# Kernel tuning notes

Measured on AMD Instinct MI355X. Metric: run time of the kernel, lower is better.

## Reference

```python
import jax, jax.numpy as jnp
import numpy as np


def _conv1x1(x, w, b):
    # x: (B,C,H,W), w: (O,C), b: (O,)  == nn.Conv2d(C,O,kernel_size=1)
    return jnp.einsum('bchw,oc->bohw', x, w) + b[None, :, None, None]


def _maxpool2(x):
    # MaxPool2d(kernel_size=2, stride=2) on NCHW
    return jax.lax.reduce_window(x, -jnp.inf, jax.lax.max,
                                 (1, 1, 2, 2), (1, 1, 2, 2), 'VALID')


def setup_inputs() -> dict:
    key = jax.random.key(0)
    ks = jax.random.split(key, 10)
    B, C, H, W = 16, 256, 64, 64
    Cs = C // 8  # channel_split = 8 -> 32
    s = 1.0 / np.sqrt(C)  # keep softmax logits well-scaled
    return {
        'x': jax.random.normal(ks[0], (B, C, H, W), dtype=jnp.float32),
        'wq': jax.random.normal(ks[1], (Cs, C), dtype=jnp.float32) * s,
        'bq': jnp.zeros((Cs,), dtype=jnp.float32),
        'wk': jax.random.normal(ks[2], (Cs, C), dtype=jnp.float32) * s,
        'bk': jnp.zeros((Cs,), dtype=jnp.float32),
        'wv': jax.random.normal(ks[3], (C, C), dtype=jnp.float32) * s,
        'bv': jnp.zeros((C,), dtype=jnp.float32),
        'wo': jax.random.normal(ks[4], (C, C), dtype=jnp.float32) * s,
        'bo': jnp.zeros((C,), dtype=jnp.float32),
        'gamma': jnp.ones((1,), dtype=jnp.float32),
    }


def reference(x, wq, bq, wk, bk, wv, bv, wo, bo, gamma):
    B, C, H, W = x.shape
    # Q: conv -> maxpool -> flatten -> (B, Np, C')
    q = _maxpool2(_conv1x1(x, wq, bq))
    Np = q.shape[2] * q.shape[3]
    q = q.reshape(B, -1, Np).transpose(0, 2, 1)          # (B, Np, C')
    # K: conv -> flatten -> (B, C', N)
    k = _conv1x1(x, wk, bk).reshape(B, -1, H * W)        # (B, C', N)
    energy = jnp.einsum('bnc,bcm->bnm', q, k)            # (B, Np, N)
    attention = jax.nn.softmax(energy, axis=-1)
    # V: conv -> maxpool -> flatten -> (B, C, Np)
    v = _maxpool2(_conv1x1(x, wv, bv)).reshape(B, C, Np)
    out = jnp.einsum('bcn,bnm->bcm', v, attention)       # (B, C, N)
    out = out.reshape(B, C, H, W)
    out = _conv1x1(out, wo, bo)
    return gamma * out + x
```

## Files before the change

### kernel.cpp

```cpp
#include <hip/hip_runtime.h>
#include <math.h>

#define Bb 16
#define Cn 256
#define Cs 32
#define Nn 4096
#define Np 1024
#define Ww 64
#define MS2 16

#define MT 64
#define NT2 128
#define PR2 (NT2 + 8)

#define PO 136
#define QKPAD 36

typedef __attribute__((ext_vector_type(8))) short short8;
typedef __attribute__((ext_vector_type(4))) float f32x4;

__device__ inline short f2bf(float f) {
    unsigned u = __builtin_bit_cast(unsigned, f);
    u += 0x7fff + ((u >> 16) & 1);
    return (short)(u >> 16);
}
__device__ inline float bf2f(short s) {
    unsigned u = ((unsigned)(unsigned short)s) << 16;
    return __builtin_bit_cast(float, u);
}
__device__ inline unsigned bfmax4(unsigned u0, unsigned u1, unsigned u2, unsigned u3) {
    float l = fmaxf(fmaxf(__builtin_bit_cast(float, u0 << 16),
                          __builtin_bit_cast(float, u1 << 16)),
                    fmaxf(__builtin_bit_cast(float, u2 << 16),
                          __builtin_bit_cast(float, u3 << 16)));
    float h = fmaxf(fmaxf(__builtin_bit_cast(float, u0 & 0xffff0000u),
                          __builtin_bit_cast(float, u1 & 0xffff0000u)),
                    fmaxf(__builtin_bit_cast(float, u2 & 0xffff0000u),
                          __builtin_bit_cast(float, u3 & 0xffff0000u)));
    return (__builtin_bit_cast(unsigned, h) & 0xffff0000u) |
           (__builtin_bit_cast(unsigned, l) >> 16);
}

__global__ void tobf_k(const float* __restrict__ in, short* __restrict__ out, int n) {
    int idx = blockIdx.x * 256 + threadIdx.x;
    if (idx < n) out[idx] = f2bf(in[idx]);
}

__global__ __launch_bounds__(256) void xpose_bf(const float* __restrict__ x,
                                                short* __restrict__ xbfT) {
    __shared__ float T[64][65];
    int lane = threadIdx.x & 63, g = threadIdx.x >> 6;
    int b = blockIdx.z, c0 = blockIdx.y * 64, m0 = blockIdx.x * 64;
    const float* xb = x + ((size_t)b * Cn + c0) * Nn + m0;
#pragma unroll
    for (int r = 0; r < 16; ++r) {
        int c_l = r * 4 + g;
        T[c_l][lane] = xb[(size_t)c_l * Nn + lane];
    }
    __syncthreads();
    short* ob = xbfT + ((size_t)b * Nn + m0) * Cn + c0;
#pragma unroll
    for (int r = 0; r < 16; ++r) {
        int m_l = r * 4 + g;
        ob[(size_t)m_l * Cn + lane] = f2bf(T[lane][m_l]);
    }
}

__global__ __launch_bounds__(256) void conv_qk_mfma(
    const short* __restrict__ xbfT, const short* __restrict__ wqBf,
    const short* __restrict__ wkBf, const float* __restrict__ bq,
    const float* __restrict__ bk, short* __restrict__ KT,
    short* __restrict__ QpT) {
    __shared__ short Tq[128 * QKPAD];
    int lane = threadIdx.x & 63;
    int wave = __builtin_amdgcn_readfirstlane(threadIdx.x >> 6);
    int l16 = lane & 15, quad = lane >> 4;
    int b = blockIdx.y;
    int h = blockIdx.x;
    int m0 = h * 128 + (wave >> 1) * 64;
    int isK = wave & 1;
    const short* wB = isK ? wkBf : wqBf;
    const float* bias = isK ? bk : bq;
    const short* Arow = wB + (size_t)l16 * Cn + quad * 8;
    const short* Brow = xbfT + ((size_t)b * Nn + m0 + l16) * Cn + quad * 8;
    f32x4 acc[2][4];
#pragma unroll
    for (int i = 0; i < 2; ++i)
#pragma unroll
        for (int j = 0; j < 4; ++j) acc[i][j] = (f32x4){0.f, 0.f, 0.f, 0.f};
    for (int kk = 0; kk < Cn; kk += 32) {
        short8 af[2], bf[4];
#pragma unroll
        for (int fo = 0; fo < 2; ++fo)
            af[fo] = *(const short8*)(Arow + (size_t)(fo * 16) * Cn + kk);
#pragma unroll
        for (int fm = 0; fm < 4; ++fm)
            bf[fm] = *(const short8*)(Brow + (size_t)(fm * 16) * Cn + kk);
#pragma unroll
        for (int fo = 0; fo < 2; ++fo)
#pragma unroll
            for (int fm = 0; fm < 4; ++fm)
                acc[fo][fm] = __builtin_amdgcn_mfma_f32_16x16x32_bf16(
                    af[fo], bf[fm], acc[fo][fm], 0, 0, 0);
    }
#pragma unroll
    for (int fo = 0; fo < 2; ++fo) {
        int c0 = fo * 16 + quad * 4;
        float b0 = bias[c0], b1 = bias[c0 + 1], b2 = bias[c0 + 2], b3 = bias[c0 + 3];
#pragma unroll
        for (int fm = 0; fm < 4; ++fm) {
            int m_rel = (wave >> 1) * 64 + fm * 16 + l16;
            unsigned lo = ((unsigned)(unsigned short)f2bf(acc[fo][fm][1] + b1) << 16) |
                          (unsigned short)f2bf(acc[fo][fm][0] + b0);
            unsigned hi = ((unsigned)(unsigned short)f2bf(acc[fo][fm][3] + b3) << 16) |
                          (unsigned short)f2bf(acc[fo][fm][2] + b2);
            if (isK) {
                int m = h * 128 + m_rel;
                *(uint2*)&KT[((size_t)b * Nn + m) * Cs + c0] = make_uint2(lo, hi);
            } else {
                *(uint2*)&Tq[m_rel * QKPAD + c0] = make_uint2(lo, hi);
            }
        }
    }
    __syncthreads();
    int pw = threadIdx.x >> 3;
    int cs = (threadIdx.x & 7) * 4;
    uint2 A0 = *(const uint2*)&Tq[(2 * pw) * QKPAD + cs];
    uint2 A1 = *(const uint2*)&Tq[(2 * pw + 1) * QKPAD + cs];
    uint2 A2 = *(const uint2*)&Tq[(64 + 2 * pw) * QKPAD + cs];
    uint2 A3 = *(const uint2*)&Tq[(64 + 2 * pw + 1) * QKPAD + cs];
    unsigned w0 = bfmax4(A0.x, A1.x, A2.x, A3.x);
    unsigned w1 = bfmax4(A0.y, A1.y, A2.y, A3.y);
    *(uint2*)&QpT[((size_t)b * Np + h * 32 + pw) * Cs + cs] = make_uint2(w0, w1);
}

__global__ __launch_bounds__(256) void conv_v_pool(
    const short* __restrict__ xbfT, const short* __restrict__ wvBf,
    const float* __restrict__ bv, short* __restrict__ VpT) {
    __shared__ short T[128 * PO];
    int lane = threadIdx.x & 63;
    int wave = __builtin_amdgcn_readfirstlane(threadIdx.x >> 6);
    int l16 = lane & 15, quad = lane >> 4;
    int b = blockIdx.z;
    int h = blockIdx.x;
    int m0 = h * 128 + (wave >> 1) * 64;
    int o0 = blockIdx.y * 128 + (wave & 1) * 64;
    const short* Arow = wvBf + (size_t)(o0 + l16) * Cn + quad * 8;
    const short* Brow = xbfT + ((size_t)b * Nn + m0 + l16) * Cn + quad * 8;
    f32x4 acc[4][4];
#pragma unroll
    for (int i = 0; i < 4; ++i)
#pragma unroll
        for (int j = 0; j < 4; ++j) acc[i][j] = (f32x4){0.f, 0.f, 0.f, 0.f};
    for (int kk = 0; kk < Cn; kk += 32) {
        short8 af[4], bf[4];
#pragma unroll
        for (int fo = 0; fo < 4; ++fo)
            af[fo] = *(const short8*)(Arow + (size_t)(fo * 16) * Cn + kk);
#pragma unroll
        for (int fm = 0; fm < 4; ++fm)
            bf[fm] = *(const short8*)(Brow + (size_t)(fm * 16) * Cn + kk);
#pragma unroll
        for (int fo = 0; fo < 4; ++fo)
#pragma unroll
            for (int fm = 0; fm < 4; ++fm)
                acc[fo][fm] = __builtin_amdgcn_mfma_f32_16x16x32_bf16(
                    af[fo], bf[fm], acc[fo][fm], 0, 0, 0);
    }
#pragma unroll
    for (int fo = 0; fo < 4; ++fo) {
        int o_loc = (wave & 1) * 64 + fo * 16 + quad * 4;
        int o_g = blockIdx.y * 128 + o_loc;
        float b0 = bv[o_g], b1 = bv[o_g + 1], b2 = bv[o_g + 2], b3 = bv[o_g + 3];
#pragma unroll
        for (int fm = 0; fm < 4; ++fm) {
            int m_rel = (wave >> 1) * 64 + fm * 16 + l16;
            unsigned lo = ((unsigned)(unsigned short)f2bf(acc[fo][fm][1] + b1) << 16) |
                          (unsigned short)f2bf(acc[fo][fm][0] + b0);
            unsigned hi = ((unsigned)(unsigned short)f2bf(acc[fo][fm][3] + b3) << 16) |
                          (unsigned short)f2bf(acc[fo][fm][2] + b2);
            *(uint2*)&T[m_rel * PO + o_loc] = make_uint2(lo, hi);
        }
    }
    __syncthreads();
#pragma unroll
    for (int rep = 0; rep < 2; ++rep) {
        int t = threadIdx.x + rep * 256;
        int cg = t & 15;
        int pw = t >> 4;
        const short* r0 = &T[(2 * pw) * PO + cg * 8];
        const short* r1 = r0 + PO;
        const short* r2 = &T[(64 + 2 * pw) * PO + cg * 8];
        const short* r3 = r2 + PO;
        short8 a = *(const short8*)r0, b8 = *(const short8*)r1;
        short8 c8 = *(const short8*)r2, d8 = *(const short8*)r3;
        short8 o8;
#pragma unroll
        for (int j = 0; j < 8; ++j) {
            float v = fmaxf(fmaxf(bf2f(a[j]), bf2f(b8[j])),
                            fmaxf(bf2f(c8[j]), bf2f(d8[j])));
            o8[j] = f2bf(v);
        }
        int n = h * 32 + pw;
        *(short8*)(VpT + ((size_t)b * Np + n) * Cn + blockIdx.y * 128 + cg * 8) = o8;
    }
}

__global__ __launch_bounds__(256) void vo_mfma(
    const short* __restrict__ VpT, const short* __restrict__ woBf,
    short* __restrict__ VoBf) {
    int lane = threadIdx.x & 63;
    int wave = __builtin_amdgcn_readfirstlane(threadIdx.x >> 6);
    int l16 = lane & 15, quad = lane >> 4;
    int b = blockIdx.z;
    int n0 = blockIdx.x * 128 + (wave >> 1) * 64;
    int o0 = blockIdx.y * 128 + (wave & 1) * 64;
    const short* Arow = woBf + (size_t)(o0 + l16) * Cn + quad * 8;
    const short* Brow = VpT + ((size_t)b * Np + n0 + l16) * Cn + quad * 8;
    f32x4 acc[4][4];
#pragma unroll
    for (int i = 0; i < 4; ++i)
#pragma unroll
        for (int j = 0; j < 4; ++j) acc[i][j] = (f32x4){0.f, 0.f, 0.f, 0.f};
    for (int kk = 0; kk < Cn; kk += 32) {
        short8 af[4], bf[4];
#pragma unroll
        for (int fo = 0; fo < 4; ++fo)
            af[fo] = *(const short8*)(Arow + (size_t)(fo * 16) * Cn + kk);
#pragma unroll
        for (int fm = 0; fm < 4; ++fm)
            bf[fm] = *(const short8*)(Brow + (size_t)(fm * 16) * Cn + kk);
#pragma unroll
        for (int fo = 0; fo < 4; ++fo)
#pragma unroll
            for (int fm = 0; fm < 4; ++fm)
                acc[fo][fm] = __builtin_amdgcn_mfma_f32_16x16x32_bf16(
                    af[fo], bf[fm], acc[fo][fm], 0, 0, 0);
    }
#pragma unroll
    for (int fo = 0; fo < 4; ++fo)
#pragma unroll
        for (int fm = 0; fm < 4; ++fm) {
            int n = n0 + fm * 16 + l16;
#pragma unroll
            for (int r = 0; r < 4; ++r) {
                int o = o0 + fo * 16 + quad * 4 + r;
                VoBf[((size_t)b * Cn + o) * Np + n] = f2bf(acc[fo][fm][r]);
            }
        }
}

__global__ __launch_bounds__(256) void rowstats_mfma(
    const short* __restrict__ KT, const short* __restrict__ QpT,
    float* __restrict__ pS) {
    int lane = threadIdx.x & 63;
    int wave = __builtin_amdgcn_readfirstlane(threadIdx.x >> 6);
    int l16 = lane & 15, quad = lane >> 4;
    int b = blockIdx.y, ms = blockIdx.z;
    int nbase = blockIdx.x * 256 + wave * 64;
    short8 af[4];
#pragma unroll
    for (int nf = 0; nf < 4; ++nf)
        af[nf] = *(const short8*)(QpT +
            ((size_t)b * Np + nbase + nf * 16 + l16) * Cs + quad * 8);
    float Sv[4][4];
#pragma unroll
    for (int nf = 0; nf < 4; ++nf)
#pragma unroll
        for (int r = 0; r < 4; ++r) Sv[nf][r] = 0.f;
    int m0 = ms * (Nn / MS2);
    for (int mm = 0; mm < Nn / MS2; mm += 16) {
        short8 bf = *(const short8*)(KT +
            ((size_t)b * Nn + m0 + mm + l16) * Cs + quad * 8);
#pragma unroll
        for (int nf = 0; nf < 4; ++nf) {
            f32x4 e = __builtin_amdgcn_mfma_f32_16x16x32_bf16(
                af[nf], bf, (f32x4){0.f, 0.f, 0.f, 0.f}, 0, 0, 0);
#pragma unroll
            for (int r = 0; r < 4; ++r)
                Sv[nf][r] += __expf(e[r] - 20.f);
        }
    }
#pragma unroll
    for (int nf = 0; nf < 4; ++nf)
#pragma unroll
        for (int r = 0; r < 4; ++r) {
            float S = Sv[nf][r];
#pragma unroll
            for (int s = 1; s <= 8; s <<= 1) S += __shfl_xor(S, s);
            Sv[nf][r] = S;
        }
    if (l16 == 0) {
#pragma unroll
        for (int nf = 0; nf < 4; ++nf)
#pragma unroll
            for (int r = 0; r < 4; ++r) {
                size_t o = ((size_t)ms * Bb + b) * Np + nbase + nf * 16 +
                           quad * 4 + r;
                pS[o] = Sv[nf][r];
            }
    }
}

__global__ void comb_k(const float* __restrict__ pS, float* __restrict__ Ae) {
    int gidx = blockIdx.x * 256 + threadIdx.x;
    int b = gidx >> 10, n = gidx & (Np - 1);
    float S = 0.f;
#pragma unroll
    for (int ms = 0; ms < MS2; ++ms)
        S += pS[((size_t)ms * Bb + b) * Np + n];
    Ae[(size_t)b * Np + n] = 20.f + __logf(S);
}

__global__ __launch_bounds__(512) void attn_out_k(
    const short* __restrict__ KT, const short* __restrict__ QpT,
    const short* __restrict__ VoBf, const float* __restrict__ Ae,
    const float* __restrict__ bo, const float* __restrict__ gamma,
    const float* __restrict__ x, float* __restrict__ out) {
    __shared__ short P[2][MT * PR2];
    int tid  = threadIdx.x;
    int lane = tid & 63;
    int wave = __builtin_amdgcn_readfirstlane(tid >> 6);
    int l16 = lane & 15, quad = lane >> 4;
    int b  = blockIdx.y;
    int m0 = blockIdx.x * MT;

    const short* QT = QpT + (size_t)b * Np * Cs;
    const short* Kb = KT + ((size_t)b * Nn + m0) * Cs;
    const short* Vb = VoBf + ((size_t)b * Cn + wave * 32) * Np;
    const float* Ab = Ae + (size_t)b * Np;

    short8 kf[4];
#pragma unroll
    for (int mf = 0; mf < 4; ++mf)
        kf[mf] = *(const short8*)(Kb + (size_t)(mf * 16 + l16) * Cs + quad * 8);

    f32x4 acc[2][4];
#pragma unroll
    for (int i = 0; i < 2; ++i)
#pragma unroll
        for (int j = 0; j < 4; ++j) acc[i][j] = (f32x4){0.f, 0.f, 0.f, 0.f};

    auto Ephase = [&](int t) {
        int buf = t & 1;
        int nb = t * NT2 + wave * 16;
        short8 qf = *(const short8*)(QT + (size_t)(nb + l16) * Cs + quad * 8);
        f32x4 av = *(const f32x4*)&Ab[nb + quad * 4];
#pragma unroll
        for (int mf = 0; mf < 4; ++mf) {
            f32x4 e = __builtin_amdgcn_mfma_f32_16x16x32_bf16(
                qf, kf[mf], (f32x4){0.f, 0.f, 0.f, 0.f}, 0, 0, 0);
            float p0 = __expf(e[0] - av[0]);
            float p1 = __expf(e[1] - av[1]);
            float p2 = __expf(e[2] - av[2]);
            float p3 = __expf(e[3] - av[3]);
            unsigned p01 = ((unsigned)(unsigned short)f2bf(p1) << 16) |
                           (unsigned short)f2bf(p0);
            unsigned p23 = ((unsigned)(unsigned short)f2bf(p3) << 16) |
                           (unsigned short)f2bf(p2);
            int m_l = mf * 16 + l16;
            int n_l = wave * 16 + quad * 4;
            *(uint2*)&P[buf][m_l * PR2 + n_l] = make_uint2(p01, p23);
        }
    };

    Ephase(0);
    __syncthreads();
    for (int t = 0; t < 8; ++t) {
        if (t < 7) Ephase(t + 1);
        const short* At = Vb + t * NT2;
        int buf = t & 1;
#pragma unroll
        for (int kk = 0; kk < NT2; kk += 32) {
            short8 bfr[4], afr[2];
#pragma unroll
            for (int fm = 0; fm < 4; ++fm)
                bfr[fm] = *(const short8*)&P[buf][(fm * 16 + l16) * PR2 + kk + quad * 8];
#pragma unroll
            for (int fo = 0; fo < 2; ++fo)
                afr[fo] = *(const short8*)(At + (size_t)(fo * 16 + l16) * Np +
                                           kk + quad * 8);
#pragma unroll
            for (int fo = 0; fo < 2; ++fo)
#pragma unroll
                for (int fm = 0; fm < 4; ++fm)
                    acc[fo][fm] = __builtin_amdgcn_mfma_f32_16x16x32_bf16(
                        afr[fo], bfr[fm], acc[fo][fm], 0, 0, 0);
        }
        __syncthreads();
    }
    float g = gamma[0];
#pragma unroll
    for (int fo = 0; fo < 2; ++fo)
#pragma unroll
        for (int fm = 0; fm < 4; ++fm) {
            int m = m0 + fm * 16 + l16;
#pragma unroll
            for (int r = 0; r < 4; ++r) {
                int o = wave * 32 + fo * 16 + quad * 4 + r;
                size_t idx = ((size_t)b * Cn + o) * Nn + m;
                out[idx] = g * (acc[fo][fm][r] + bo[o]) + x[idx];
            }
        }
}

extern "C" void kernel_launch(void* const* d_in, const int* in_sizes, int n_in,
                              void* d_out, int out_size, void* d_ws, size_t ws_size,
                              hipStream_t stream) {
    (void)in_sizes; (void)n_in; (void)out_size; (void)ws_size;
    const float* x     = (const float*)d_in[0];
    const float* wq    = (const float*)d_in[1];
    const float* bq    = (const float*)d_in[2];
    const float* wk    = (const float*)d_in[3];
    const float* bk    = (const float*)d_in[4];
    const float* wv    = (const float*)d_in[5];
    const float* bv    = (const float*)d_in[6];
    const float* wo    = (const float*)d_in[7];
    const float* bo    = (const float*)d_in[8];
    const float* gamma = (const float*)d_in[9];
    float* out = (float*)d_out;

    float* ws = (float*)d_ws;
    size_t off = 0;
    short* xbfT = (short*)(ws + off); off += (size_t)Bb * Nn * Cn / 2;
    short* VpT  = (short*)(ws + off); off += (size_t)Bb * Np * Cn / 2;
    short* VoBf = (short*)(ws + off); off += (size_t)Bb * Cn * Np / 2;
    short* KT   = (short*)(ws + off); off += (size_t)Bb * Nn * Cs / 2;
    short* QpT  = (short*)(ws + off); off += (size_t)Bb * Np * Cs / 2;
    float* pS   = ws + off;           off += (size_t)MS2 * Bb * Np;
    float* Ae   = ws + off;           off += (size_t)Bb * Np;
    short* wqBf = (short*)(ws + off); off += (size_t)Cs * Cn / 2;
    short* wkBf = (short*)(ws + off); off += (size_t)Cs * Cn / 2;
    short* wvBf = (short*)(ws + off); off += (size_t)Cn * Cn / 2;
    short* woBf = (short*)(ws + off); off += (size_t)Cn * Cn / 2;

    tobf_k<<<dim3((Cs * Cn + 255) / 256), 256, 0, stream>>>(wq, wqBf, Cs * Cn);
    tobf_k<<<dim3((Cs * Cn + 255) / 256), 256, 0, stream>>>(wk, wkBf, Cs * Cn);
    tobf_k<<<dim3(Cn * Cn / 256), 256, 0, stream>>>(wv, wvBf, Cn * Cn);
    tobf_k<<<dim3(Cn * Cn / 256), 256, 0, stream>>>(wo, woBf, Cn * Cn);

    xpose_bf<<<dim3(Nn / 64, Cn / 64, Bb), 256, 0, stream>>>(x, xbfT);

    conv_qk_mfma<<<dim3(Nn / 128, Bb), 256, 0, stream>>>(xbfT, wqBf, wkBf,
                                                         bq, bk, KT, QpT);

    conv_v_pool<<<dim3(Nn / 128, Cn / 128, Bb), 256, 0, stream>>>(xbfT, wvBf, bv, VpT);

    rowstats_mfma<<<dim3(Np / 256, Bb, MS2), 256, 0, stream>>>(KT, QpT, pS);
    comb_k<<<dim3(Bb * Np / 256), 256, 0, stream>>>(pS, Ae);

    vo_mfma<<<dim3(Np / 128, Cn / 128, Bb), 256, 0, stream>>>(VpT, woBf, VoBf);

    attn_out_k<<<dim3(Nn / MT, Bb), 512, 0, stream>>>(KT, QpT, VoBf, Ae,
                                                      bo, gamma, x, out);
}
```

Before: 284.4 us.

## Merge independent launches, fold log2e into Wq, use exp2 and packed bf16 converts

Four weight-conversion kernels are merged into one launch. The Q/K and V convolutions now run in a single grid dispatched by block index, and so do rowstats and vo_mfma. This removes launch gaps and lets independent work share the device. Wq and bq are prescaled by log2(e) so softmax can use the hardware exp2/log2 instructions, and float-to-bf16 packing uses v_cvt_pk_bf16_f32. Rounding from prescaling Wq in bf16 changes numerics slightly.

```diff
diff --git a/kernel.cpp b/kernel.cpp
--- a/kernel.cpp
+++ b/kernel.cpp
@@ -16,8 +16,14 @@
 #define PO 136
 #define QKPAD 36
 
+#define C20L 28.8539008f
+#define L2E  1.44269504f
+
 typedef __attribute__((ext_vector_type(8))) short short8;
 typedef __attribute__((ext_vector_type(4))) float f32x4;
+
+__device__ inline float fexp2(float x) { return __builtin_amdgcn_exp2f(x); }
+__device__ inline float flog2(float x) { return __builtin_amdgcn_logf(x); }
 
 __device__ inline short f2bf(float f) {
     unsigned u = __builtin_bit_cast(unsigned, f);
@@ -27,6 +33,11 @@
 __device__ inline float bf2f(short s) {
     unsigned u = ((unsigned)(unsigned short)s) << 16;
     return __builtin_bit_cast(float, u);
+}
+__device__ inline unsigned pk2bf(float lo, float hi) {
+    unsigned r;
+    asm("v_cvt_pk_bf16_f32 %0, %1, %2" : "=v"(r) : "v"(lo), "v"(hi));
+    return r;
 }
 __device__ inline unsigned bfmax4(unsigned u0, unsigned u1, unsigned u2, unsigned u3) {
     float l = fmaxf(fmaxf(__builtin_bit_cast(float, u0 << 16),
@@ -41,9 +52,15 @@
            (__builtin_bit_cast(unsigned, l) >> 16);
 }
 
-__global__ void tobf_k(const float* __restrict__ in, short* __restrict__ out, int n) {
+__global__ void wprep_k(const float* __restrict__ wq, const float* __restrict__ wk,
+                        const float* __restrict__ wv, const float* __restrict__ wo,
+                        short* __restrict__ wqBf, short* __restrict__ wkBf,
+                        short* __restrict__ wvBf, short* __restrict__ woBf) {
     int idx = blockIdx.x * 256 + threadIdx.x;
-    if (idx < n) out[idx] = f2bf(in[idx]);
+    if (idx < 8192)        wqBf[idx] = f2bf(wq[idx] * L2E);
+    else if (idx < 16384)  wkBf[idx - 8192] = f2bf(wk[idx - 8192]);
+    else if (idx < 81920)  wvBf[idx - 16384] = f2bf(wv[idx - 16384]);
+    else if (idx < 147456) woBf[idx - 81920] = f2bf(wo[idx - 81920]);
 }
 
 __global__ __launch_bounds__(256) void xpose_bf(const float* __restrict__ x,
@@ -66,238 +83,231 @@
     }
 }
 
-__global__ __launch_bounds__(256) void conv_qk_mfma(
+__global__ __launch_bounds__(256) void convs_k(
     const short* __restrict__ xbfT, const short* __restrict__ wqBf,
     const short* __restrict__ wkBf, const float* __restrict__ bq,
-    const float* __restrict__ bk, short* __restrict__ KT,
-    short* __restrict__ QpT) {
-    __shared__ short Tq[128 * QKPAD];
-    int lane = threadIdx.x & 63;
-    int wave = __builtin_amdgcn_readfirstlane(threadIdx.x >> 6);
-    int l16 = lane & 15, quad = lane >> 4;
-    int b = blockIdx.y;
-    int h = blockIdx.x;
-    int m0 = h * 128 + (wave >> 1) * 64;
-    int isK = wave & 1;
-    const short* wB = isK ? wkBf : wqBf;
-    const float* bias = isK ? bk : bq;
-    const short* Arow = wB + (size_t)l16 * Cn + quad * 8;
-    const short* Brow = xbfT + ((size_t)b * Nn + m0 + l16) * Cn + quad * 8;
-    f32x4 acc[2][4];
-#pragma unroll
-    for (int i = 0; i < 2; ++i)
-#pragma unroll
-        for (int j = 0; j < 4; ++j) acc[i][j] = (f32x4){0.f, 0.f, 0.f, 0.f};
-    for (int kk = 0; kk < Cn; kk += 32) {
-        short8 af[2], bf[4];
-#pragma unroll
-        for (int fo = 0; fo < 2; ++fo)
-            af[fo] = *(const short8*)(Arow + (size_t)(fo * 16) * Cn + kk);
-#pragma unroll
-        for (int fm = 0; fm < 4; ++fm)
-            bf[fm] = *(const short8*)(Brow + (size_t)(fm * 16) * Cn + kk);
-#pragma unroll
-        for (int fo = 0; fo < 2; ++fo)
-#pragma unroll
-            for (int fm = 0; fm < 4; ++fm)
-                acc[fo][fm] = __builtin_amdgcn_mfma_f32_16x16x32_bf16(
-                    af[fo], bf[fm], acc[fo][fm], 0, 0, 0);
-    }
-#pragma unroll
-    for (int fo = 0; fo < 2; ++fo) {
-        int c0 = fo * 16 + quad * 4;
-        float b0 = bias[c0], b1 = bias[c0 + 1], b2 = bias[c0 + 2], b3 = bias[c0 + 3];
-#pragma unroll
-        for (int fm = 0; fm < 4; ++fm) {
-            int m_rel = (wave >> 1) * 64 + fm * 16 + l16;
-            unsigned lo = ((unsigned)(unsigned short)f2bf(acc[fo][fm][1] + b1) << 16) |
-                          (unsigned short)f2bf(acc[fo][fm][0] + b0);
-            unsigned hi = ((unsigned)(unsigned short)f2bf(acc[fo][fm][3] + b3) << 16) |
-                          (unsigned short)f2bf(acc[fo][fm][2] + b2);
-            if (isK) {
-                int m = h * 128 + m_rel;
-                *(uint2*)&KT[((size_t)b * Nn + m) * Cs + c0] = make_uint2(lo, hi);
-            } else {
-                *(uint2*)&Tq[m_rel * QKPAD + c0] = make_uint2(lo, hi);
-            }
-        }
-    }
-    __syncthreads();
-    int pw = threadIdx.x >> 3;
-    int cs = (threadIdx.x & 7) * 4;
-    uint2 A0 = *(const uint2*)&Tq[(2 * pw) * QKPAD + cs];
-    uint2 A1 = *(const uint2*)&Tq[(2 * pw + 1) * QKPAD + cs];
-    uint2 A2 = *(const uint2*)&Tq[(64 + 2 * pw) * QKPAD + cs];
-    uint2 A3 = *(const uint2*)&Tq[(64 + 2 * pw + 1) * QKPAD + cs];
-    unsigned w0 = bfmax4(A0.x, A1.x, A2.x, A3.x);
-    unsigned w1 = bfmax4(A0.y, A1.y, A2.y, A3.y);
-    *(uint2*)&QpT[((size_t)b * Np + h * 32 + pw) * Cs + cs] = make_uint2(w0, w1);
-}
-
-__global__ __launch_bounds__(256) void conv_v_pool(
-    const short* __restrict__ xbfT, const short* __restrict__ wvBf,
-    const float* __restrict__ bv, short* __restrict__ VpT) {
+    const float* __restrict__ bk, const short* __restrict__ wvBf,
+    const float* __restrict__ bv, short* __restrict__ KT,
+    short* __restrict__ QpT, short* __restrict__ VpT) {
     __shared__ short T[128 * PO];
     int lane = threadIdx.x & 63;
     int wave = __builtin_amdgcn_readfirstlane(threadIdx.x >> 6);
     int l16 = lane & 15, quad = lane >> 4;
-    int b = blockIdx.z;
-    int h = blockIdx.x;
-    int m0 = h * 128 + (wave >> 1) * 64;
-    int o0 = blockIdx.y * 128 + (wave & 1) * 64;
-    const short* Arow = wvBf + (size_t)(o0 + l16) * Cn + quad * 8;
-    const short* Brow = xbfT + ((size_t)b * Nn + m0 + l16) * Cn + quad * 8;
-    f32x4 acc[4][4];
-#pragma unroll
-    for (int i = 0; i < 4; ++i)
-#pragma unroll
-        for (int j = 0; j < 4; ++j) acc[i][j] = (f32x4){0.f, 0.f, 0.f, 0.f};
-    for (int kk = 0; kk < Cn; kk += 32) {
-        short8 af[4], bf[4];
-#pragma unroll
-        for (int fo = 0; fo < 4; ++fo)
-            af[fo] = *(const short8*)(Arow + (size_t)(fo * 16) * Cn + kk);
-#pragma unroll
-        for (int fm = 0; fm < 4; ++fm)
-            bf[fm] = *(const short8*)(Brow + (size_t)(fm * 16) * Cn + kk);
-#pragma unroll
-        for (int fo = 0; fo < 4; ++fo)
+    int bid = blockIdx.x;
+
+    if (bid < 512) {
+        int h = bid & 31, b = bid >> 5;
+        int m0 = h * 128 + (wave >> 1) * 64;
+        int isK = wave & 1;
+        const short* wB = isK ? wkBf : wqBf;
+        const float* bias = isK ? bk : bq;
+        float bs = isK ? 1.f : L2E;
+        const short* Arow = wB + (size_t)l16 * Cn + quad * 8;
+        const short* Brow = xbfT + ((size_t)b * Nn + m0 + l16) * Cn + quad * 8;
+        f32x4 acc[2][4];
+#pragma unroll
+        for (int i = 0; i < 2; ++i)
+#pragma unroll
+            for (int j = 0; j < 4; ++j) acc[i][j] = (f32x4){0.f, 0.f, 0.f, 0.f};
+        for (int kk = 0; kk < Cn; kk += 32) {
+            short8 af[2], bf[4];
+#pragma unroll
+            for (int fo = 0; fo < 2; ++fo)
+                af[fo] = *(const short8*)(Arow + (size_t)(fo * 16) * Cn + kk);
 #pragma unroll
             for (int fm = 0; fm < 4; ++fm)
-                acc[fo][fm] = __builtin_amdgcn_mfma_f32_16x16x32_bf16(
-                    af[fo], bf[fm], acc[fo][fm], 0, 0, 0);
+                bf[fm] = *(const short8*)(Brow + (size_t)(fm * 16) * Cn + kk);
+#pragma unroll
+            for (int fo = 0; fo < 2; ++fo)
+#pragma unroll
+                for (int fm = 0; fm < 4; ++fm)
+                    acc[fo][fm] = __builtin_amdgcn_mfma_f32_16x16x32_bf16(
+                        af[fo], bf[fm], acc[fo][fm], 0, 0, 0);
+        }
+#pragma unroll
+        for (int fo = 0; fo < 2; ++fo) {
+            int c0 = fo * 16 + quad * 4;
+            float b0 = bias[c0] * bs, b1 = bias[c0 + 1] * bs;
+            float b2 = bias[c0 + 2] * bs, b3 = bias[c0 + 3] * bs;
+#pragma unroll
+            for (int fm = 0; fm < 4; ++fm) {
+                int m_rel = (wave >> 1) * 64 + fm * 16 + l16;
+                unsigned lo = pk2bf(acc[fo][fm][0] + b0, acc[fo][fm][1] + b1);
+                unsigned hi = pk2bf(acc[fo][fm][2] + b2, acc[fo][fm][3] + b3);
+                if (isK) {
+                    int m = h * 128 + m_rel;
+                    *(uint2*)&KT[((size_t)b * Nn + m) * Cs + c0] = make_uint2(lo, hi);
+                } else {
+                    *(uint2*)&T[m_rel * QKPAD + c0] = make_uint2(lo, hi);
+                }
+            }
+        }
+        __syncthreads();
+        int pw = threadIdx.x >> 3;
+        int cs = (threadIdx.x & 7) * 4;
+        uint2 A0 = *(const uint2*)&T[(2 * pw) * QKPAD + cs];
+        uint2 A1 = *(const uint2*)&T[(2 * pw + 1) * QKPAD + cs];
+        uint2 A2 = *(const uint2*)&T[(64 + 2 * pw) * QKPAD + cs];
+        uint2 A3 = *(const uint2*)&T[(64 + 2 * pw + 1) * QKPAD + cs];
+        unsigned w0 = bfmax4(A0.x, A1.x, A2.x, A3.x);
+        unsigned w1 = bfmax4(A0.y, A1.y, A2.y, A3.y);
+        *(uint2*)&QpT[((size_t)b * Np + h * 32 + pw) * Cs + cs] = make_uint2(w0, w1);
+    } else {
+        bid -= 512;
+        int h = bid & 31, oy = (bid >> 5) & 1, b = bid >> 6;
+        int m0 = h * 128 + (wave >> 1) * 64;
+        int o0 = oy * 128 + (wave & 1) * 64;
+        const short* Arow = wvBf + (size_t)(o0 + l16) * Cn + quad * 8;
+        const short* Brow = xbfT + ((size_t)b * Nn + m0 + l16) * Cn + quad * 8;
+        f32x4 acc[4][4];
+#pragma unroll
+        for (int i = 0; i < 4; ++i)
+#pragma unroll
+            for (int j = 0; j < 4; ++j) acc[i][j] = (f32x4){0.f, 0.f, 0.f, 0.f};
+        for (int kk = 0; kk < Cn; kk += 32) {
+            short8 af[4], bf[4];
+#pragma unroll
+            for (int fo = 0; fo < 4; ++fo)
+                af[fo] = *(const short8*)(Arow + (size_t)(fo * 16) * Cn + kk);
+#pragma unroll
+            for (int fm = 0; fm < 4; ++fm)
+                bf[fm] = *(const short8*)(Brow + (size_t)(fm * 16) * Cn + kk);
+#pragma unroll
+            for (int fo = 0; fo < 4; ++fo)
+#pragma unroll
+                for (int fm = 0; fm < 4; ++fm)
+                    acc[fo][fm] = __builtin_amdgcn_mfma_f32_16x16x32_bf16(
+                        af[fo], bf[fm], acc[fo][fm], 0, 0, 0);
+        }
+#pragma unroll
+        for (int fo = 0; fo < 4; ++fo) {
+            int o_loc = (wave & 1) * 64 + fo * 16 + quad * 4;
+            int o_g = oy * 128 + o_loc;
+            float b0 = bv[o_g], b1 = bv[o_g + 1], b2 = bv[o_g + 2], b3 = bv[o_g + 3];
+#pragma unroll
+            for (int fm = 0; fm < 4; ++fm) {
+                int m_rel = (wave >> 1) * 64 + fm * 16 + l16;
+                unsigned lo = pk2bf(acc[fo][fm][0] + b0, acc[fo][fm][1] + b1);
+                unsigned hi = pk2bf(acc[fo][fm][2] + b2, acc[fo][fm][3] + b3);
+                *(uint2*)&T[m_rel * PO + o_loc] = make_uint2(lo, hi);
+            }
+        }
+        __syncthreads();
+#pragma unroll
+        for (int rep = 0; rep < 2; ++rep) {
+            int t = threadIdx.x + rep * 256;
+            int cg = t & 15;
+            int pw = t >> 4;
+            const short* r0 = &T[(2 * pw) * PO + cg * 8];
+            const short* r1 = r0 + PO;
+            const short* r2 = &T[(64 + 2 * pw) * PO + cg * 8];
+            const short* r3 = r2 + PO;
+            short8 a = *(const short8*)r0, b8 = *(const short8*)r1;
+            short8 c8 = *(const short8*)r2, d8 = *(const short8*)r3;
+            short8 o8;
+#pragma unroll
+            for (int j = 0; j < 8; ++j) {
+                float v = fmaxf(fmaxf(bf2f(a[j]), bf2f(b8[j])),
+                                fmaxf(bf2f(c8[j]), bf2f(d8[j])));
+                o8[j] = f2bf(v);
+            }
+            int n = h * 32 + pw;
+            *(short8*)(VpT + ((size_t)b * Np + n) * Cn + oy * 128 + cg * 8) = o8;
+        }
     }
-#pragma unroll
-    for (int fo = 0; fo < 4; ++fo) {
-        int o_loc = (wave & 1) * 64 + fo * 16 + quad * 4;
-        int o_g = blockIdx.y * 128 + o_loc;
-        float b0 = bv[o_g], b1 = bv[o_g + 1], b2 = bv[o_g + 2], b3 = bv[o_g + 3];
-#pragma unroll
-        for (int fm = 0; fm < 4; ++fm) {
-            int m_rel = (wave >> 1) * 64 + fm * 16 + l16;
-            unsigned lo = ((unsigned)(unsigned short)f2bf(acc[fo][fm][1] + b1) << 16) |
-                          (unsigned short)f2bf(acc[fo][fm][0] + b0);
-            unsigned hi = ((unsigned)(unsigned short)f2bf(acc[fo][fm][3] + b3) << 16) |
-                          (unsigned short)f2bf(acc[fo][fm][2] + b2);
-            *(uint2*)&T[m_rel * PO + o_loc] = make_uint2(lo, hi);
-        }
-    }
-    __syncthreads();
-#pragma unroll
-    for (int rep = 0; rep < 2; ++rep) {
-        int t = threadIdx.x + rep * 256;
-        int cg = t & 15;
-        int pw = t >> 4;
-        const short* r0 = &T[(2 * pw) * PO + cg * 8];
-        const short* r1 = r0 + PO;
-        const short* r2 = &T[(64 + 2 * pw) * PO + cg * 8];
-        const short* r3 = r2 + PO;
-        short8 a = *(const short8*)r0, b8 = *(const short8*)r1;
-        short8 c8 = *(const short8*)r2, d8 = *(const short8*)r3;
-        short8 o8;
-#pragma unroll
-        for (int j = 0; j < 8; ++j) {
-            float v = fmaxf(fmaxf(bf2f(a[j]), bf2f(b8[j])),
-                            fmaxf(bf2f(c8[j]), bf2f(d8[j])));
-            o8[j] = f2bf(v);
-        }
-        int n = h * 32 + pw;
-        *(short8*)(VpT + ((size_t)b * Np + n) * Cn + blockIdx.y * 128 + cg * 8) = o8;
-    }
-}
-
-__global__ __launch_bounds__(256) void vo_mfma(
-    const short* __restrict__ VpT, const short* __restrict__ woBf,
-    short* __restrict__ VoBf) {
+}
+
+__global__ __launch_bounds__(256) void stats_vo_k(
+    const short* __restrict__ KT, const short* __restrict__ QpT,
+    float* __restrict__ pS, const short* __restrict__ VpT,
+    const short* __restrict__ woBf, short* __restrict__ VoBf) {
     int lane = threadIdx.x & 63;
     int wave = __builtin_amdgcn_readfirstlane(threadIdx.x >> 6);
     int l16 = lane & 15, quad = lane >> 4;
-    int b = blockIdx.z;
-    int n0 = blockIdx.x * 128 + (wave >> 1) * 64;
-    int o0 = blockIdx.y * 128 + (wave & 1) * 64;
-    const short* Arow = woBf + (size_t)(o0 + l16) * Cn + quad * 8;
-    const short* Brow = VpT + ((size_t)b * Np + n0 + l16) * Cn + quad * 8;
-    f32x4 acc[4][4];
-#pragma unroll
-    for (int i = 0; i < 4; ++i)
-#pragma unroll
-        for (int j = 0; j < 4; ++j) acc[i][j] = (f32x4){0.f, 0.f, 0.f, 0.f};
-    for (int kk = 0; kk < Cn; kk += 32) {
-        short8 af[4], bf[4];
+    int bid = blockIdx.x;
+
+    if (bid < 1024) {
+        int nx = bid & 3, b = (bid >> 2) & 15, ms = bid >> 6;
+        int nbase = nx * 256 + wave * 64;
+        short8 af[4];
+#pragma unroll
+        for (int nf = 0; nf < 4; ++nf)
+            af[nf] = *(const short8*)(QpT +
+                ((size_t)b * Np + nbase + nf * 16 + l16) * Cs + quad * 8);
+        float Sv[4][4];
+#pragma unroll
+        for (int nf = 0; nf < 4; ++nf)
+#pragma unroll
+            for (int r = 0; r < 4; ++r) Sv[nf][r] = 0.f;
+        int m0 = ms * (Nn / MS2);
+        for (int mm = 0; mm < Nn / MS2; mm += 16) {
+            short8 bf = *(const short8*)(KT +
+                ((size_t)b * Nn + m0 + mm + l16) * Cs + quad * 8);
+#pragma unroll
+            for (int nf = 0; nf < 4; ++nf) {
+                f32x4 e = __builtin_amdgcn_mfma_f32_16x16x32_bf16(
+                    af[nf], bf, (f32x4){0.f, 0.f, 0.f, 0.f}, 0, 0, 0);
+#pragma unroll
+                for (int r = 0; r < 4; ++r)
+                    Sv[nf][r] += fexp2(e[r] - C20L);
+            }
+        }
+#pragma unroll
+        for (int nf = 0; nf < 4; ++nf)
+#pragma unroll
+            for (int r = 0; r < 4; ++r) {
+                float S = Sv[nf][r];
+#pragma unroll
+                for (int s = 1; s <= 8; s <<= 1) S += __shfl_xor(S, s);
+                Sv[nf][r] = S;
+            }
+        if (l16 == 0) {
+#pragma unroll
+            for (int nf = 0; nf < 4; ++nf)
+#pragma unroll
+                for (int r = 0; r < 4; ++r) {
+                    size_t o = ((size_t)ms * Bb + b) * Np + nbase + nf * 16 +
+                               quad * 4 + r;
+                    pS[o] = Sv[nf][r];
+                }
+        }
+    } else {
+        bid -= 1024;
+        int nx = bid & 7, oy = (bid >> 3) & 1, b = bid >> 4;
+        int n0 = nx * 128 + (wave >> 1) * 64;
+        int o0 = oy * 128 + (wave & 1) * 64;
+        const short* Arow = woBf + (size_t)(o0 + l16) * Cn + quad * 8;
+        const short* Brow = VpT + ((size_t)b * Np + n0 + l16) * Cn + quad * 8;
+        f32x4 acc[4][4];
+#pragma unroll
+        for (int i = 0; i < 4; ++i)
+#pragma unroll
+            for (int j = 0; j < 4; ++j) acc[i][j] = (f32x4){0.f, 0.f, 0.f, 0.f};
+        for (int kk = 0; kk < Cn; kk += 32) {
+            short8 af[4], bf[4];
+#pragma unroll
+            for (int fo = 0; fo < 4; ++fo)
+                af[fo] = *(const short8*)(Arow + (size_t)(fo * 16) * Cn + kk);
+#pragma unroll
+            for (int fm = 0; fm < 4; ++fm)
+                bf[fm] = *(const short8*)(Brow + (size_t)(fm * 16) * Cn + kk);
+#pragma unroll
+            for (int fo = 0; fo < 4; ++fo)
+#pragma unroll
+                for (int fm = 0; fm < 4; ++fm)
+                    acc[fo][fm] = __builtin_amdgcn_mfma_f32_16x16x32_bf16(
+                        af[fo], bf[fm], acc[fo][fm], 0, 0, 0);
+        }
 #pragma unroll
         for (int fo = 0; fo < 4; ++fo)
-            af[fo] = *(const short8*)(Arow + (size_t)(fo * 16) * Cn + kk);
-#pragma unroll
-        for (int fm = 0; fm < 4; ++fm)
-            bf[fm] = *(const short8*)(Brow + (size_t)(fm * 16) * Cn + kk);
-#pragma unroll
-        for (int fo = 0; fo < 4; ++fo)
-#pragma unroll
-            for (int fm = 0; fm < 4; ++fm)
-                acc[fo][fm] = __builtin_amdgcn_mfma_f32_16x16x32_bf16(
-                    af[fo], bf[fm], acc[fo][fm], 0, 0, 0);
-    }
-#pragma unroll
-    for (int fo = 0; fo < 4; ++fo)
-#pragma unroll
-        for (int fm = 0; fm < 4; ++fm) {
-            int n = n0 + fm * 16 + l16;
-#pragma unroll
-            for (int r = 0; r < 4; ++r) {
-                int o = o0 + fo * 16 + quad * 4 + r;
-                VoBf[((size_t)b * Cn + o) * Np + n] = f2bf(acc[fo][fm][r]);
-            }
-        }
-}
-
-__global__ __launch_bounds__(256) void rowstats_mfma(
-    const short* __restrict__ KT, const short* __restrict__ QpT,
-    float* __restrict__ pS) {
-    int lane = threadIdx.x & 63;
-    int wave = __builtin_amdgcn_readfirstlane(threadIdx.x >> 6);
-    int l16 = lane & 15, quad = lane >> 4;
-    int b = blockIdx.y, ms = blockIdx.z;
-    int nbase = blockIdx.x * 256 + wave * 64;
-    short8 af[4];
-#pragma unroll
-    for (int nf = 0; nf < 4; ++nf)
-        af[nf] = *(const short8*)(QpT +
-            ((size_t)b * Np + nbase + nf * 16 + l16) * Cs + quad * 8);
-    float Sv[4][4];
-#pragma unroll
-    for (int nf = 0; nf < 4; ++nf)
-#pragma unroll
-        for (int r = 0; r < 4; ++r) Sv[nf][r] = 0.f;
-    int m0 = ms * (Nn / MS2);
-    for (int mm = 0; mm < Nn / MS2; mm += 16) {
-        short8 bf = *(const short8*)(KT +
-            ((size_t)b * Nn + m0 + mm + l16) * Cs + quad * 8);
-#pragma unroll
-        for (int nf = 0; nf < 4; ++nf) {
-            f32x4 e = __builtin_amdgcn_mfma_f32_16x16x32_bf16(
-                af[nf], bf, (f32x4){0.f, 0.f, 0.f, 0.f}, 0, 0, 0);
-#pragma unroll
-            for (int r = 0; r < 4; ++r)
-                Sv[nf][r] += __expf(e[r] - 20.f);
-        }
-    }
-#pragma unroll
-    for (int nf = 0; nf < 4; ++nf)
-#pragma unroll
-        for (int r = 0; r < 4; ++r) {
-            float S = Sv[nf][r];
-#pragma unroll
-            for (int s = 1; s <= 8; s <<= 1) S += __shfl_xor(S, s);
-            Sv[nf][r] = S;
-        }
-    if (l16 == 0) {
-#pragma unroll
-        for (int nf = 0; nf < 4; ++nf)
-#pragma unroll
-            for (int r = 0; r < 4; ++r) {
-                size_t o = ((size_t)ms * Bb + b) * Np + nbase + nf * 16 +
-                           quad * 4 + r;
-                pS[o] = Sv[nf][r];
+#pragma unroll
+            for (int fm = 0; fm < 4; ++fm) {
+                int n = n0 + fm * 16 + l16;
+#pragma unroll
+                for (int r = 0; r < 4; ++r) {
+                    int o = o0 + fo * 16 + quad * 4 + r;
+                    VoBf[((size_t)b * Cn + o) * Np + n] = f2bf(acc[fo][fm][r]);
+                }
             }
     }
 }
@@ -309,7 +319,7 @@
 #pragma unroll
     for (int ms = 0; ms < MS2; ++ms)
         S += pS[((size_t)ms * Bb + b) * Np + n];
-    Ae[(size_t)b * Np + n] = 20.f + __logf(S);
+    Ae[(size_t)b * Np + n] = C20L + flog2(S);
 }
 
 __global__ __launch_bounds__(512) void attn_out_k(
@@ -350,14 +360,12 @@
         for (int mf = 0; mf < 4; ++mf) {
             f32x4 e = __builtin_amdgcn_mfma_f32_16x16x32_bf16(
                 qf, kf[mf], (f32x4){0.f, 0.f, 0.f, 0.f}, 0, 0, 0);
-            float p0 = __expf(e[0] - av[0]);
-            float p1 = __expf(e[1] - av[1]);
-            float p2 = __expf(e[2] - av[2]);
-            float p3 = __expf(e[3] - av[3]);
-            unsigned p01 = ((unsigned)(unsigned short)f2bf(p1) << 16) |
-                           (unsigned short)f2bf(p0);
-            unsigned p23 = ((unsigned)(unsigned short)f2bf(p3) << 16) |
-                           (unsigned short)f2bf(p2);
+            float p0 = fexp2(e[0] - av[0]);
+            float p1 = fexp2(e[1] - av[1]);
+            float p2 = fexp2(e[2] - av[2]);
+            float p3 = fexp2(e[3] - av[3]);
+            unsigned p01 = pk2bf(p0, p1);
+            unsigned p23 = pk2bf(p2, p3);
             int m_l = mf * 16 + l16;
             int n_l = wave * 16 + quad * 4;
             *(uint2*)&P[buf][m_l * PR2 + n_l] = make_uint2(p01, p23);
@@ -434,22 +442,16 @@
     short* wvBf = (short*)(ws + off); off += (size_t)Cn * Cn / 2;
     short* woBf = (short*)(ws + off); off += (size_t)Cn * Cn / 2;
 
-    tobf_k<<<dim3((Cs * Cn + 255) / 256), 256, 0, stream>>>(wq, wqBf, Cs * Cn);
-    tobf_k<<<dim3((Cs * Cn + 255) / 256), 256, 0, stream>>>(wk, wkBf, Cs * Cn);
-    tobf_k<<<dim3(Cn * Cn / 256), 256, 0, stream>>>(wv, wvBf, Cn * Cn);
-    tobf_k<<<dim3(Cn * Cn / 256), 256, 0, stream>>>(wo, woBf, Cn * Cn);
+    wprep_k<<<dim3(576), 256, 0, stream>>>(wq, wk, wv, wo, wqBf, wkBf, wvBf, woBf);
 
     xpose_bf<<<dim3(Nn / 64, Cn / 64, Bb), 256, 0, stream>>>(x, xbfT);
 
-    conv_qk_mfma<<<dim3(Nn / 128, Bb), 256, 0, stream>>>(xbfT, wqBf, wkBf,
-                                                         bq, bk, KT, QpT);
-
-    conv_v_pool<<<dim3(Nn / 128, Cn / 128, Bb), 256, 0, stream>>>(xbfT, wvBf, bv, VpT);
-
-    rowstats_mfma<<<dim3(Np / 256, Bb, MS2), 256, 0, stream>>>(KT, QpT, pS);
+    convs_k<<<dim3(512 + 1024), 256, 0, stream>>>(xbfT, wqBf, wkBf, bq, bk,
+                                                  wvBf, bv, KT, QpT, VpT);
+
+    stats_vo_k<<<dim3(1024 + 256), 256, 0, stream>>>(KT, QpT, pS, VpT, woBf, VoBf);
+
     comb_k<<<dim3(Bb * Np / 256), 256, 0, stream>>>(pS, Ae);
-
-    vo_mfma<<<dim3(Np / 128, Cn / 128, Bb), 256, 0, stream>>>(VpT, woBf, VoBf);
 
     attn_out_k<<<dim3(Nn / MT, Bb), 512, 0, stream>>>(KT, QpT, VoBf, Ae,
                                                       bo, gamma, x, out);
```

After: 271.1 us. -4.7%, faster.
